# Performance work log

Measured on AMD Instinct MI355X. Metric: run time of the kernel, lower is better.

The kernel has to match this reference:

```python
import jax, jax.numpy as jnp
import numpy as np
import math

B_SZ, T_LEN = 2, 1024
D_MODEL, D_STATE, D_CONV, EXPAND = 1024, 16, 4, 2
D_INNER = EXPAND * D_MODEL            # 2048
DT_RANK = math.ceil(D_MODEL / 16)     # 64


def setup_inputs() -> dict:
    key = jax.random.key(0)
    ks = jax.random.split(key, 10)
    f32 = jnp.float32
    x = jax.random.normal(ks[0], (B_SZ, T_LEN, D_MODEL), f32)
    norm_w = jnp.ones((D_MODEL,), f32)
    in_proj_w = jax.random.normal(ks[1], (2 * D_INNER, D_MODEL), f32) / np.sqrt(D_MODEL)
    conv_w = jax.random.uniform(ks[2], (D_INNER, 1, D_CONV), f32, -0.5, 0.5)
    conv_b = jax.random.uniform(ks[3], (D_INNER,), f32, -0.5, 0.5)
    x_proj_w = jax.random.normal(ks[4], (DT_RANK + 2 * D_STATE, D_INNER), f32) / np.sqrt(D_INNER)
    dt_std = DT_RANK ** (-0.5)
    dt_proj_w = jax.random.uniform(ks[5], (D_INNER, DT_RANK), f32, -dt_std, dt_std)
    # dt bias init: softplus(bias) lands in [dt_min, dt_max]
    dt = jnp.exp(jax.random.uniform(ks[6], (D_INNER,), f32) * (np.log(0.1) - np.log(0.001)) + np.log(0.001))
    dt_proj_b = dt + jnp.log(-jnp.expm1(-dt))
    A_log = jnp.log(jnp.tile(jnp.arange(1, D_STATE + 1, dtype=f32)[None, :], (D_INNER, 1)))
    D_param = jnp.ones((D_INNER,), f32)
    out_proj_w = jax.random.normal(ks[7], (D_MODEL, D_INNER), f32) / np.sqrt(D_INNER)
    return {"x": x, "norm_w": norm_w, "in_proj_w": in_proj_w, "conv_w": conv_w,
            "conv_b": conv_b, "x_proj_w": x_proj_w, "dt_proj_w": dt_proj_w,
            "dt_proj_b": dt_proj_b, "A_log": A_log, "D_param": D_param,
            "out_proj_w": out_proj_w}


def _mamba_forward(x, norm_w, in_proj_w, conv_w, conv_b, x_proj_w,
                   dt_proj_w, dt_proj_b, A_log, D_param, out_proj_w):
    residual = x
    # RMSNorm (torch nn.RMSNorm, eps=None -> finfo eps)
    eps = jnp.finfo(x.dtype).eps
    xn = x * jax.lax.rsqrt(jnp.mean(x * x, axis=-1, keepdims=True) + eps) * norm_w
    # input projection -> ssm stream + gate
    xz = xn @ in_proj_w.T                     # [B,T,2*d_inner]
    x_s, z = xz[..., :D_INNER], xz[..., D_INNER:]
    # causal depthwise conv1d (pad left d_conv-1, matches padding=d_conv-1 then [:T])
    u = jax.lax.conv_general_dilated(
        x_s.transpose(0, 2, 1), conv_w, window_strides=(1,),
        padding=[(D_CONV - 1, 0)], dimension_numbers=("NCH", "OIH", "NCH"),
        feature_group_count=D_INNER) + conv_b[None, :, None]
    u = jax.nn.silu(u).transpose(0, 2, 1)     # [B,T,d_inner]
    # input-dependent SSM params
    x_dbc = u @ x_proj_w.T
    dt_raw = x_dbc[..., :DT_RANK]
    B_ssm = x_dbc[..., DT_RANK:DT_RANK + D_STATE]
    C_ssm = x_dbc[..., DT_RANK + D_STATE:]
    delta = jax.nn.softplus(dt_raw @ dt_proj_w.T + dt_proj_b)   # [B,T,d_inner]
    A = -jnp.exp(A_log)                                         # [d_inner,d_state]
    # discretize
    dA = jnp.exp(jnp.einsum("bti,is->btis", delta, A))          # [B,T,i,s]
    dBu = jnp.einsum("bti,bts->btis", delta * u, B_ssm)         # [B,T,i,s]
    # sequential scan over time (lax.scan, carry h [B,i,s])
    def step(h, inp):
        dA_t, dBu_t, C_t = inp
        h = dA_t * h + dBu_t
        y_t = jnp.einsum("bis,bs->bi", h, C_t)
        return h, y_t
    h0 = jnp.zeros((x.shape[0], D_INNER, D_STATE), x.dtype)
    _, ys = jax.lax.scan(step, h0,
                         (dA.transpose(1, 0, 2, 3), dBu.transpose(1, 0, 2, 3),
                          C_ssm.transpose(1, 0, 2)))
    y = ys.transpose(1, 0, 2) + u * D_param                     # [B,T,d_inner]
    y = y * jax.nn.silu(z)
    return y @ out_proj_w.T + residual


def reference(x, norm_w, in_proj_w, conv_w, conv_b, x_proj_w,
              dt_proj_w, dt_proj_b, A_log, D_param, out_proj_w):
    return _mamba_forward(x, norm_w, in_proj_w, conv_w, conv_b, x_proj_w,
                          dt_proj_w, dt_proj_b, A_log, D_param, out_proj_w)
```

## Files before the change

kernel.cpp:

```cpp
#include <hip/hip_runtime.h>
#include <math.h>

#define B_SZ 2
#define T_LEN 1024
#define D_MODEL 1024
#define D_STATE 16
#define D_INNER 2048
#define DT_RANK 64
#define NTOK (B_SZ * T_LEN)
#define XPROJ_OUT 96
#define XPROJ_LD 128
#define NCHUNK 32
#define CHUNK_L (T_LEN / NCHUNK)
#define NSPLIT 16

typedef __attribute__((ext_vector_type(8))) short bf16x8;
typedef __attribute__((ext_vector_type(4))) float f32x4;

__device__ __forceinline__ float sigmoidf_(float x) { return 1.f / (1.f + __expf(-x)); }

__device__ __forceinline__ unsigned f2bf_u(float f) {
    unsigned u = __float_as_uint(f);
    return (u + 0x7FFFu + ((u >> 16) & 1u)) >> 16;
}
__device__ __forceinline__ float bf2f(unsigned short u) {
    return __uint_as_float((unsigned)u << 16);
}

__device__ __forceinline__ void gload_lds16(const void* g, void* l) {
    __builtin_amdgcn_global_load_lds((const __attribute__((address_space(1))) unsigned*)g,
                                     (__attribute__((address_space(3))) unsigned*)l,
                                     16, 0, 0);
}

__global__ __launch_bounds__(256) void k_prep(const float* __restrict__ x,
                                              const float* __restrict__ norm_w,
                                              const float* __restrict__ w_in,
                                              const float* __restrict__ w_out,
                                              const float* __restrict__ w_x,
                                              const float* __restrict__ w_dt,
                                              unsigned short* __restrict__ xn,
                                              unsigned* __restrict__ wib,
                                              unsigned* __restrict__ wob,
                                              unsigned* __restrict__ wxb,
                                              unsigned* __restrict__ wdtb) {
    __shared__ float red[4];
    int blk = blockIdx.x;
    if (blk < 2048) {
        const float* xr = x + (size_t)blk * D_MODEL;
        int i = threadIdx.x * 4;
        float4 xv = *(const float4*)(xr + i);
        float s = xv.x * xv.x + xv.y * xv.y + xv.z * xv.z + xv.w * xv.w;
#pragma unroll
        for (int m = 1; m <= 32; m <<= 1) s += __shfl_xor(s, m);
        if ((threadIdx.x & 63) == 0) red[threadIdx.x >> 6] = s;
        __syncthreads();
        float tot = red[0] + red[1] + red[2] + red[3];
        float scale = rsqrtf(tot * (1.f / D_MODEL) + 1.1920929e-07f);
        float4 wv = *(const float4*)(norm_w + i);
        uint2 o;
        o.x = f2bf_u(xv.x * scale * wv.x) | (f2bf_u(xv.y * scale * wv.y) << 16);
        o.y = f2bf_u(xv.z * scale * wv.z) | (f2bf_u(xv.w * scale * wv.w) << 16);
        *(uint2*)(xn + (size_t)blk * D_MODEL + i) = o;
        return;
    }
    blk -= 2048;
    const float* src;
    unsigned* dst;
    int lidx;
    if (blk < 2048) {
        src = w_in; dst = wib; lidx = blk * 256 + threadIdx.x;
    } else if (blk < 3072) {
        src = w_out; dst = wob; lidx = (blk - 2048) * 256 + threadIdx.x;
    } else if (blk < 3200) {
        dst = wxb; lidx = (blk - 3072) * 256 + threadIdx.x;
        if (lidx * 8 >= 96 * 2048) {
            uint4 z = {0, 0, 0, 0};
            ((uint4*)dst)[lidx] = z;
            return;
        }
        src = w_x;
    } else {
        src = w_dt; dst = wdtb; lidx = (blk - 3200) * 256 + threadIdx.x;
    }
    float4 a = ((const float4*)src)[lidx * 2];
    float4 b = ((const float4*)src)[lidx * 2 + 1];
    uint4 o;
    o.x = f2bf_u(a.x) | (f2bf_u(a.y) << 16);
    o.y = f2bf_u(a.z) | (f2bf_u(a.w) << 16);
    o.z = f2bf_u(b.x) | (f2bf_u(b.y) << 16);
    o.w = f2bf_u(b.z) | (f2bf_u(b.w) << 16);
    ((uint4*)dst)[lidx] = o;
}


template <int BN, int CW, int EPI>
__global__ __launch_bounds__(256) void gemm_bf16(const unsigned short* __restrict__ A,
                                                 const unsigned short* __restrict__ B,
                                                 void* __restrict__ Cv, int ldc, int K,
                                                 const float* __restrict__ res) {
    constexpr int RW = 4 / CW;
    constexpr int MI = (128 / RW) / 16;
    constexpr int NJ = (BN / CW) / 16;
    __shared__ __align__(16) unsigned short As[2][128 * 64];
    __shared__ __align__(16) unsigned short Bs[2][BN * 64];
    int tid = threadIdx.x;
    int lane = tid & 63, wv = tid >> 6;
    int wr = wv / CW, wc = wv % CW;
    int lm = lane & 15, q = lane >> 4;
    int sw = lm & 7;
    int m0 = blockIdx.x * 128, n0 = blockIdx.y * BN;
    f32x4 acc[MI][NJ] = {};

    auto stage = [&](int bufi, int k0) {
#pragma unroll
        for (int it = 0; it < 4; ++it) {
            int chunk = it * 256 + tid;
            int cc = (chunk & 7) ^ ((chunk >> 3) & 7);
            const unsigned short* g = A + (size_t)(m0 + (chunk >> 3)) * K + k0 + cc * 8;
            char* l = (char*)As[bufi] + (it * 256 + wv * 64) * 16 + lane * 16;
            gload_lds16(g, l);
        }
#pragma unroll
        for (int it = 0; it < BN / 32; ++it) {
            int chunk = it * 256 + tid;
            int cc = (chunk & 7) ^ ((chunk >> 3) & 7);
            const unsigned short* g = B + (size_t)(n0 + (chunk >> 3)) * K + k0 + cc * 8;
            char* l = (char*)Bs[bufi] + (it * 256 + wv * 64) * 16 + lane * 16;
            gload_lds16(g, l);
        }
    };

    stage(0, 0);
    __syncthreads();
    int cur = 0;
    for (int k0 = 0; k0 < K; k0 += 64) {
        if (k0 + 64 < K) stage(cur ^ 1, k0 + 64);
        const unsigned short* Ac = As[cur];
        const unsigned short* Bc = Bs[cur];
#pragma unroll
        for (int h = 0; h < 2; ++h) {
            bf16x8 af[MI], bfr[NJ];
#pragma unroll
            for (int i = 0; i < MI; ++i)
                af[i] = *(const bf16x8*)(Ac + (wr * MI * 16 + i * 16 + lm) * 64 +
                                         (((h << 2) + q) ^ sw) * 8);
#pragma unroll
            for (int j = 0; j < NJ; ++j)
                bfr[j] = *(const bf16x8*)(Bc + (wc * NJ * 16 + j * 16 + lm) * 64 +
                                          (((h << 2) + q) ^ sw) * 8);
#pragma unroll
            for (int i = 0; i < MI; ++i)
#pragma unroll
                for (int j = 0; j < NJ; ++j)
                    acc[i][j] = __builtin_amdgcn_mfma_f32_16x16x32_bf16(af[i], bfr[j], acc[i][j], 0, 0, 0);
        }
        __syncthreads();
        cur ^= 1;
    }
#pragma unroll
    for (int i = 0; i < MI; ++i) {
#pragma unroll
        for (int j = 0; j < NJ; ++j) {
#pragma unroll
            for (int r = 0; r < 4; ++r) {
                int row = m0 + wr * MI * 16 + i * 16 + q * 4 + r;
                int col = n0 + wc * NJ * 16 + j * 16 + lm;
                float v = acc[i][j][r];
                if (EPI == 0) {
                    ((float*)Cv)[(size_t)row * ldc + col] = v + res[(size_t)row * ldc + col];
                } else if (EPI == 1) {
                    v += res[col];
                    v = (v > 20.f) ? v : log1pf(__expf(v));
                    ((unsigned short*)Cv)[(size_t)row * ldc + col] = (unsigned short)f2bf_u(v);
                } else {
                    if (n0 >= D_INNER) v = v * sigmoidf_(v);
                    ((unsigned short*)Cv)[(size_t)row * ldc + col] = (unsigned short)f2bf_u(v);
                }
            }
        }
    }
}

__global__ __launch_bounds__(256) void xproj_gemm(const unsigned short* __restrict__ A,
                                                  const unsigned short* __restrict__ B,
                                                  unsigned short* __restrict__ part) {
    constexpr int MI = 4, NJ = 4;
    __shared__ __align__(16) unsigned short As[2][128 * 64];
    __shared__ __align__(16) unsigned short Bs[2][128 * 64];
    int tid = threadIdx.x;
    int lane = tid & 63, wv = tid >> 6;
    int wr = wv >> 1, wc = wv & 1;
    int lm = lane & 15, q = lane >> 4;
    int sw = lm & 7;
    int m0 = blockIdx.x * 128;
    int kbase = blockIdx.y * 128;
    f32x4 acc[MI][NJ] = {};

    auto stage = [&](int bufi, int k0) {
#pragma unroll
        for (int it = 0; it < 4; ++it) {
            int chunk = it * 256 + tid;
            int cc = (chunk & 7) ^ ((chunk >> 3) & 7);
            const unsigned short* g = A + (size_t)(m0 + (chunk >> 3)) * D_INNER + k0 + cc * 8;
            char* l = (char*)As[bufi] + (it * 256 + wv * 64) * 16 + lane * 16;
            gload_lds16(g, l);
        }
#pragma unroll
        for (int it = 0; it < 4; ++it) {
            int chunk = it * 256 + tid;
            int cc = (chunk & 7) ^ ((chunk >> 3) & 7);
            const unsigned short* g = B + (size_t)(chunk >> 3) * D_INNER + k0 + cc * 8;
            char* l = (char*)Bs[bufi] + (it * 256 + wv * 64) * 16 + lane * 16;
            gload_lds16(g, l);
        }
    };

    stage(0, kbase);
    __syncthreads();
    for (int ks = 0; ks < 2; ++ks) {
        if (ks == 0) stage(1, kbase + 64);
        const unsigned short* Ac = As[ks];
        const unsigned short* Bc = Bs[ks];
#pragma unroll
        for (int h = 0; h < 2; ++h) {
            bf16x8 af[MI], bfr[NJ];
#pragma unroll
            for (int i = 0; i < MI; ++i)
                af[i] = *(const bf16x8*)(Ac + (wr * 64 + i * 16 + lm) * 64 + (((h << 2) + q) ^ sw) * 8);
#pragma unroll
            for (int j = 0; j < NJ; ++j)
                bfr[j] = *(const bf16x8*)(Bc + (wc * 64 + j * 16 + lm) * 64 + (((h << 2) + q) ^ sw) * 8);
#pragma unroll
            for (int i = 0; i < MI; ++i)
#pragma unroll
                for (int j = 0; j < NJ; ++j)
                    acc[i][j] = __builtin_amdgcn_mfma_f32_16x16x32_bf16(af[i], bfr[j], acc[i][j], 0, 0, 0);
        }
        __syncthreads();
    }
    unsigned short* dst = part + (size_t)blockIdx.y * (NTOK * XPROJ_LD);
#pragma unroll
    for (int i = 0; i < MI; ++i)
#pragma unroll
        for (int j = 0; j < NJ; ++j)
#pragma unroll
            for (int r = 0; r < 4; ++r) {
                int row = m0 + wr * 64 + i * 16 + q * 4 + r;
                int col = wc * 64 + j * 16 + lm;
                dst[(size_t)row * XPROJ_LD + col] = (unsigned short)f2bf_u(acc[i][j][r]);
            }
}

__global__ __launch_bounds__(256) void k_xred(const unsigned short* __restrict__ part,
                                              float* __restrict__ dbc,
                                              unsigned short* __restrict__ dtrawb) {
    int idx4 = blockIdx.x * 256 + threadIdx.x;
    float s0 = 0.f, s1 = 0.f, s2 = 0.f, s3 = 0.f;
#pragma unroll
    for (int sp = 0; sp < NSPLIT; ++sp) {
        uint2 v = *(const uint2*)(part + (size_t)sp * (NTOK * XPROJ_LD) + idx4 * 4);
        s0 += __uint_as_float(v.x << 16);
        s1 += __uint_as_float(v.x & 0xFFFF0000u);
        s2 += __uint_as_float(v.y << 16);
        s3 += __uint_as_float(v.y & 0xFFFF0000u);
    }
    float4 sv = {s0, s1, s2, s3};
    *(float4*)(dbc + idx4 * 4) = sv;
    int col = (idx4 * 4) & (XPROJ_LD - 1);
    if (col < DT_RANK) {
        int row = (idx4 * 4) >> 7;
        uint2 o;
        o.x = f2bf_u(s0) | (f2bf_u(s1) << 16);
        o.y = f2bf_u(s2) | (f2bf_u(s3) << 16);
        *(uint2*)(dtrawb + (size_t)row * DT_RANK + col) = o;
    }
}

__global__ __launch_bounds__(256) void k_conv(const unsigned short* __restrict__ xz,
                                              const float* __restrict__ cw,
                                              const float* __restrict__ cb,
                                              unsigned short* __restrict__ ub) {
    int idx = blockIdx.x * 256 + threadIdx.x;
    int c4 = (idx & (D_INNER / 4 - 1)) * 4;
    int t = (idx >> 9) & (T_LEN - 1);
    int b = idx >> 19;
    const unsigned short* xs = xz + (size_t)b * T_LEN * 2 * D_INNER + c4;
    float4 w[4];
#pragma unroll
    for (int i = 0; i < 4; ++i) w[i] = ((const float4*)cw)[c4 + i];
    float4 cbv = *(const float4*)(cb + c4);
    float s[4] = {cbv.x, cbv.y, cbv.z, cbv.w};
#pragma unroll
    for (int k = 0; k < 4; ++k) {
        int tt = t - 3 + k;
        if (tt >= 0) {
            ushort4 xv = *(const ushort4*)(xs + (size_t)tt * 2 * D_INNER);
            float fx0 = bf2f(xv.x), fx1 = bf2f(xv.y), fx2 = bf2f(xv.z), fx3 = bf2f(xv.w);
            float w0 = (k == 0) ? w[0].x : (k == 1) ? w[0].y : (k == 2) ? w[0].z : w[0].w;
            float w1 = (k == 0) ? w[1].x : (k == 1) ? w[1].y : (k == 2) ? w[1].z : w[1].w;
            float w2 = (k == 0) ? w[2].x : (k == 1) ? w[2].y : (k == 2) ? w[2].z : w[2].w;
            float w3 = (k == 0) ? w[3].x : (k == 1) ? w[3].y : (k == 2) ? w[3].z : w[3].w;
            s[0] = fmaf(fx0, w0, s[0]);
            s[1] = fmaf(fx1, w1, s[1]);
            s[2] = fmaf(fx2, w2, s[2]);
            s[3] = fmaf(fx3, w3, s[3]);
        }
    }
    ushort4 o;
    o.x = (unsigned short)f2bf_u(s[0] * sigmoidf_(s[0]));
    o.y = (unsigned short)f2bf_u(s[1] * sigmoidf_(s[1]));
    o.z = (unsigned short)f2bf_u(s[2] * sigmoidf_(s[2]));
    o.w = (unsigned short)f2bf_u(s[3] * sigmoidf_(s[3]));
    *(ushort4*)(ub + (size_t)(b * T_LEN + t) * D_INNER + c4) = o;
}

__global__ __launch_bounds__(256) void k_scan1(const unsigned short* __restrict__ delta,
                                               const unsigned short* __restrict__ ub,
                                               const float* __restrict__ dbc,
                                               const float* __restrict__ A_log,
                                               float* __restrict__ Pbuf,
                                               float* __restrict__ Hbuf) {
    int tid = threadIdx.x;
    int c = blockIdx.x * 256 + tid;
    int b = blockIdx.y >> 5, chunk = blockIdx.y & 31;
    int t0 = chunk * CHUNK_L;
    __shared__ float bc[CHUNK_L][32];
    {
        int t = tid >> 3, col = (tid & 7) * 4;
        const float* src = dbc + ((size_t)b * T_LEN + t0 + t) * XPROJ_LD + DT_RANK + col;
        *(float4*)&bc[t][col] = *(const float4*)src;
    }
    __syncthreads();
    float A[16];
#pragma unroll
    for (int s4 = 0; s4 < 4; ++s4) {
        float4 av = *(const float4*)(A_log + (size_t)c * D_STATE + s4 * 4);
        A[s4 * 4 + 0] = -__expf(av.x);
        A[s4 * 4 + 1] = -__expf(av.y);
        A[s4 * 4 + 2] = -__expf(av.z);
        A[s4 * 4 + 3] = -__expf(av.w);
    }
    const unsigned short* dp = delta + ((size_t)b * T_LEN + t0) * D_INNER + c;
    const unsigned short* up = ub + ((size_t)b * T_LEN + t0) * D_INNER + c;
    float h[16] = {};
    float sumd = 0.f;
#pragma unroll 4
    for (int t = 0; t < CHUNK_L; ++t) {
        float dv = bf2f(dp[(size_t)t * D_INNER]);
        float uv = bf2f(up[(size_t)t * D_INNER]);
        float du = dv * uv;
        sumd += dv;
#pragma unroll
        for (int s = 0; s < 16; ++s) {
            float da = __expf(dv * A[s]);
            h[s] = fmaf(da, h[s], du * bc[t][s]);
        }
    }
    size_t o = ((size_t)((b * NCHUNK + chunk) * D_INNER) + c) * 16;
#pragma unroll
    for (int s4 = 0; s4 < 4; ++s4) {
        float4 hv = {h[s4 * 4], h[s4 * 4 + 1], h[s4 * 4 + 2], h[s4 * 4 + 3]};
        *(float4*)(Hbuf + o + s4 * 4) = hv;
        float4 pv = {__expf(A[s4 * 4] * sumd), __expf(A[s4 * 4 + 1] * sumd),
                     __expf(A[s4 * 4 + 2] * sumd), __expf(A[s4 * 4 + 3] * sumd)};
        *(float4*)(Pbuf + o + s4 * 4) = pv;
    }
}

__global__ __launch_bounds__(256) void k_scan2(const float* __restrict__ Pbuf,
                                               const float* __restrict__ Hbuf,
                                               float* __restrict__ Sbuf) {
    int idx = blockIdx.x * 256 + threadIdx.x;
    int b = idx >> 15, r = idx & 32767;
    size_t base = (size_t)b * NCHUNK * (D_INNER * 16) + r;
    float p[NCHUNK], hl[NCHUNK];
#pragma unroll
    for (int ch = 0; ch < NCHUNK; ++ch) {
        size_t o = base + (size_t)ch * (D_INNER * 16);
        p[ch] = Pbuf[o];
        hl[ch] = Hbuf[o];
    }
    float h = 0.f;
#pragma unroll
    for (int ch = 0; ch < NCHUNK; ++ch) {
        Sbuf[base + (size_t)ch * (D_INNER * 16)] = h;
        h = fmaf(p[ch], h, hl[ch]);
    }
}

__global__ __launch_bounds__(256) void k_scan3(const unsigned short* __restrict__ delta,
                                               const unsigned short* __restrict__ ub,
                                               const float* __restrict__ dbc,
                                               const unsigned short* __restrict__ xz,
                                               const float* __restrict__ A_log,
                                               const float* __restrict__ Dp,
                                               const float* __restrict__ Sbuf,
                                               unsigned short* __restrict__ yb) {
    int tid = threadIdx.x;
    int c = blockIdx.x * 256 + tid;
    int b = blockIdx.y >> 5, chunk = blockIdx.y & 31;
    int t0 = chunk * CHUNK_L;
    __shared__ float bc[CHUNK_L][32];
    {
        int t = tid >> 3, col = (tid & 7) * 4;
        const float* src = dbc + ((size_t)b * T_LEN + t0 + t) * XPROJ_LD + DT_RANK + col;
        *(float4*)&bc[t][col] = *(const float4*)src;
    }
    __syncthreads();
    float A[16];
#pragma unroll
    for (int s4 = 0; s4 < 4; ++s4) {
        float4 av = *(const float4*)(A_log + (size_t)c * D_STATE + s4 * 4);
        A[s4 * 4 + 0] = -__expf(av.x);
        A[s4 * 4 + 1] = -__expf(av.y);
        A[s4 * 4 + 2] = -__expf(av.z);
        A[s4 * 4 + 3] = -__expf(av.w);
    }
    float Dc = Dp[c];
    float h[16];
    size_t ho = ((size_t)((b * NCHUNK + chunk) * D_INNER) + c) * 16;
#pragma unroll
    for (int s4 = 0; s4 < 4; ++s4) {
        float4 hv = *(const float4*)(Sbuf + ho + s4 * 4);
        h[s4 * 4] = hv.x; h[s4 * 4 + 1] = hv.y; h[s4 * 4 + 2] = hv.z; h[s4 * 4 + 3] = hv.w;
    }
    const unsigned short* dp = delta + ((size_t)b * T_LEN + t0) * D_INNER + c;
    const unsigned short* up = ub + ((size_t)b * T_LEN + t0) * D_INNER + c;
    const unsigned short* zp = xz + ((size_t)b * T_LEN + t0) * 2 * D_INNER + D_INNER + c;
    unsigned short* yp = yb + ((size_t)b * T_LEN + t0) * D_INNER + c;
#pragma unroll 2
    for (int t = 0; t < CHUNK_L; ++t) {
        float dv = bf2f(dp[(size_t)t * D_INNER]);
        float uv = bf2f(up[(size_t)t * D_INNER]);
        float sz = bf2f(zp[(size_t)t * 2 * D_INNER]);
        float du = dv * uv;
        float y = Dc * uv;
#pragma unroll
        for (int s = 0; s < 16; ++s) {
            float da = __expf(dv * A[s]);
            h[s] = fmaf(da, h[s], du * bc[t][s]);
            y = fmaf(h[s], bc[t][16 + s], y);
        }
        yp[(size_t)t * D_INNER] = (unsigned short)f2bf_u(y * sz);
    }
}

extern "C" void kernel_launch(void* const* d_in, const int* in_sizes, int n_in,
                              void* d_out, int out_size, void* d_ws, size_t ws_size,
                              hipStream_t stream) {
    const float* x         = (const float*)d_in[0];
    const float* norm_w    = (const float*)d_in[1];
    const float* in_proj_w = (const float*)d_in[2];
    const float* conv_w    = (const float*)d_in[3];
    const float* conv_b    = (const float*)d_in[4];
    const float* x_proj_w  = (const float*)d_in[5];
    const float* dt_proj_w = (const float*)d_in[6];
    const float* dt_proj_b = (const float*)d_in[7];
    const float* A_log     = (const float*)d_in[8];
    const float* D_param   = (const float*)d_in[9];
    const float* out_proj_w= (const float*)d_in[10];
    float* out = (float*)d_out;

    float* ws = (float*)d_ws;
    unsigned short* xzb    = (unsigned short*)(ws);
    unsigned short* ub     = (unsigned short*)(ws + 4194304);
    unsigned short* yb     = (unsigned short*)(ws + 6291456);
    unsigned short* partb  = (unsigned short*)(ws + 8388608);
    float*          dbc    = ws + 12582912;
    unsigned short* deltab = (unsigned short*)(ws + 12845056);
    float*          Pbuf   = ws + 14942208;
    float*          Hbuf   = ws + 17039360;
    float*          Sbuf   = ws + 19136512;
    unsigned short* wib    = (unsigned short*)(ws + 21233664);
    unsigned short* wob    = (unsigned short*)(ws + 23330816);
    unsigned short* wxb    = (unsigned short*)(ws + 24379392);
    unsigned short* wdtb   = (unsigned short*)(ws + 24510464);
    unsigned short* dtrawb = (unsigned short*)(ws + 24576000);
    unsigned short* xnb    = (unsigned short*)(ws + 24641536);

    k_prep<<<5312, 256, 0, stream>>>(x, norm_w, in_proj_w, out_proj_w, x_proj_w, dt_proj_w,
                                     xnb, (unsigned*)wib, (unsigned*)wob, (unsigned*)wxb,
                                     (unsigned*)wdtb);
    gemm_bf16<128, 2, 3><<<dim3(NTOK / 128, 4096 / 128), 256, 0, stream>>>(
        xnb, wib, xzb, 2 * D_INNER, D_MODEL, nullptr);
    k_conv<<<(NTOK * D_INNER / 4) / 256, 256, 0, stream>>>(xzb, conv_w, conv_b, ub);
    xproj_gemm<<<dim3(NTOK / 128, NSPLIT), 256, 0, stream>>>(ub, wxb, partb);
    k_xred<<<(NTOK * XPROJ_LD) / 1024, 256, 0, stream>>>(partb, dbc, dtrawb);
    gemm_bf16<64, 1, 1><<<dim3(NTOK / 128, D_INNER / 64), 256, 0, stream>>>(
        dtrawb, wdtb, deltab, D_INNER, DT_RANK, dt_proj_b);
    k_scan1<<<dim3(D_INNER / 256, B_SZ * NCHUNK), 256, 0, stream>>>(deltab, ub, dbc, A_log,
                                                                    Pbuf, Hbuf);
    k_scan2<<<(B_SZ * D_INNER * D_STATE) / 256, 256, 0, stream>>>(Pbuf, Hbuf, Sbuf);
    k_scan3<<<dim3(D_INNER / 256, B_SZ * NCHUNK), 256, 0, stream>>>(deltab, ub, dbc, xzb, A_log,
                                                                    D_param, Sbuf, yb);
    gemm_bf16<64, 2, 0><<<dim3(NTOK / 128, D_MODEL / 64), 256, 0, stream>>>(
        yb, wob, (void*)out, D_MODEL, D_INNER, x);

    (void)in_sizes; (void)n_in; (void)out_size; (void)ws_size;
}
```

Baseline: 252.7 us.

## Split SSM state across 4 threads per channel and stage scan inputs in LDS

The chunked scan kernels now assign four threads per channel, each owning four of the sixteen state dimensions, which gives four times as many blocks and far fewer registers per thread. Delta, u and gate values for the chunk are loaded once into shared memory with 16-byte vector loads, replacing per-timestep strided 2-byte global loads. In the output kernel the partial y values are reduced with lane shuffles and written back through shared memory as coalesced vector stores. This adds shuffle and LDS traffic per timestep, and redundant exp work for delta in exchange for higher occupancy and better memory coalescing.

```diff
diff --git a/kernel.cpp b/kernel.cpp
--- a/kernel.cpp
+++ b/kernel.cpp
@@ -322,50 +322,47 @@
                                                float* __restrict__ Pbuf,
                                                float* __restrict__ Hbuf) {
     int tid = threadIdx.x;
-    int c = blockIdx.x * 256 + tid;
+    int cl = tid >> 2, sq = tid & 3;
+    int c0 = blockIdx.x * 64;
+    int c = c0 + cl;
     int b = blockIdx.y >> 5, chunk = blockIdx.y & 31;
     int t0 = chunk * CHUNK_L;
     __shared__ float bc[CHUNK_L][32];
+    __shared__ __align__(16) unsigned short sd[CHUNK_L][64];
+    __shared__ __align__(16) unsigned short su[CHUNK_L][64];
     {
         int t = tid >> 3, col = (tid & 7) * 4;
         const float* src = dbc + ((size_t)b * T_LEN + t0 + t) * XPROJ_LD + DT_RANK + col;
         *(float4*)&bc[t][col] = *(const float4*)src;
     }
+    {
+        int r = tid >> 3, c8 = (tid & 7) * 8;
+        const unsigned short* dp0 = delta + ((size_t)b * T_LEN + t0) * D_INNER + c0;
+        const unsigned short* up0 = ub + ((size_t)b * T_LEN + t0) * D_INNER + c0;
+        *(uint4*)&sd[r][c8] = *(const uint4*)(dp0 + (size_t)r * D_INNER + c8);
+        *(uint4*)&su[r][c8] = *(const uint4*)(up0 + (size_t)r * D_INNER + c8);
+    }
     __syncthreads();
-    float A[16];
-#pragma unroll
-    for (int s4 = 0; s4 < 4; ++s4) {
-        float4 av = *(const float4*)(A_log + (size_t)c * D_STATE + s4 * 4);
-        A[s4 * 4 + 0] = -__expf(av.x);
-        A[s4 * 4 + 1] = -__expf(av.y);
-        A[s4 * 4 + 2] = -__expf(av.z);
-        A[s4 * 4 + 3] = -__expf(av.w);
-    }
-    const unsigned short* dp = delta + ((size_t)b * T_LEN + t0) * D_INNER + c;
-    const unsigned short* up = ub + ((size_t)b * T_LEN + t0) * D_INNER + c;
-    float h[16] = {};
-    float sumd = 0.f;
+    float4 av = *(const float4*)(A_log + (size_t)c * D_STATE + sq * 4);
+    float A0 = -__expf(av.x), A1 = -__expf(av.y), A2 = -__expf(av.z), A3 = -__expf(av.w);
+    float h0 = 0.f, h1 = 0.f, h2 = 0.f, h3 = 0.f, sumd = 0.f;
 #pragma unroll 4
     for (int t = 0; t < CHUNK_L; ++t) {
-        float dv = bf2f(dp[(size_t)t * D_INNER]);
-        float uv = bf2f(up[(size_t)t * D_INNER]);
+        float dv = bf2f(sd[t][cl]);
+        float uv = bf2f(su[t][cl]);
         float du = dv * uv;
         sumd += dv;
-#pragma unroll
-        for (int s = 0; s < 16; ++s) {
-            float da = __expf(dv * A[s]);
-            h[s] = fmaf(da, h[s], du * bc[t][s]);
-        }
-    }
-    size_t o = ((size_t)((b * NCHUNK + chunk) * D_INNER) + c) * 16;
-#pragma unroll
-    for (int s4 = 0; s4 < 4; ++s4) {
-        float4 hv = {h[s4 * 4], h[s4 * 4 + 1], h[s4 * 4 + 2], h[s4 * 4 + 3]};
-        *(float4*)(Hbuf + o + s4 * 4) = hv;
-        float4 pv = {__expf(A[s4 * 4] * sumd), __expf(A[s4 * 4 + 1] * sumd),
-                     __expf(A[s4 * 4 + 2] * sumd), __expf(A[s4 * 4 + 3] * sumd)};
-        *(float4*)(Pbuf + o + s4 * 4) = pv;
-    }
+        float4 Bv = *(const float4*)&bc[t][sq * 4];
+        h0 = fmaf(__expf(dv * A0), h0, du * Bv.x);
+        h1 = fmaf(__expf(dv * A1), h1, du * Bv.y);
+        h2 = fmaf(__expf(dv * A2), h2, du * Bv.z);
+        h3 = fmaf(__expf(dv * A3), h3, du * Bv.w);
+    }
+    size_t o = ((size_t)((b * NCHUNK + chunk) * D_INNER) + c) * 16 + sq * 4;
+    float4 hv = {h0, h1, h2, h3};
+    *(float4*)(Hbuf + o) = hv;
+    float4 pv = {__expf(A0 * sumd), __expf(A1 * sumd), __expf(A2 * sumd), __expf(A3 * sumd)};
+    *(float4*)(Pbuf + o) = pv;
 }
 
 __global__ __launch_bounds__(256) void k_scan2(const float* __restrict__ Pbuf,
@@ -398,51 +395,59 @@
                                                const float* __restrict__ Sbuf,
                                                unsigned short* __restrict__ yb) {
     int tid = threadIdx.x;
-    int c = blockIdx.x * 256 + tid;
+    int cl = tid >> 2, sq = tid & 3;
+    int c0 = blockIdx.x * 64;
+    int c = c0 + cl;
     int b = blockIdx.y >> 5, chunk = blockIdx.y & 31;
     int t0 = chunk * CHUNK_L;
     __shared__ float bc[CHUNK_L][32];
+    __shared__ __align__(16) unsigned short sd[CHUNK_L][64];
+    __shared__ __align__(16) unsigned short su[CHUNK_L][64];
+    __shared__ __align__(16) unsigned short szy[CHUNK_L][64];
     {
         int t = tid >> 3, col = (tid & 7) * 4;
         const float* src = dbc + ((size_t)b * T_LEN + t0 + t) * XPROJ_LD + DT_RANK + col;
         *(float4*)&bc[t][col] = *(const float4*)src;
     }
+    int r = tid >> 3, c8 = (tid & 7) * 8;
+    {
+        const unsigned short* dp0 = delta + ((size_t)b * T_LEN + t0) * D_INNER + c0;
+        const unsigned short* up0 = ub + ((size_t)b * T_LEN + t0) * D_INNER + c0;
+        const unsigned short* zp0 = xz + ((size_t)b * T_LEN + t0) * 2 * D_INNER + D_INNER + c0;
+        *(uint4*)&sd[r][c8] = *(const uint4*)(dp0 + (size_t)r * D_INNER + c8);
+        *(uint4*)&su[r][c8] = *(const uint4*)(up0 + (size_t)r * D_INNER + c8);
+        *(uint4*)&szy[r][c8] = *(const uint4*)(zp0 + (size_t)r * 2 * D_INNER + c8);
+    }
     __syncthreads();
-    float A[16];
-#pragma unroll
-    for (int s4 = 0; s4 < 4; ++s4) {
-        float4 av = *(const float4*)(A_log + (size_t)c * D_STATE + s4 * 4);
-        A[s4 * 4 + 0] = -__expf(av.x);
-        A[s4 * 4 + 1] = -__expf(av.y);
-        A[s4 * 4 + 2] = -__expf(av.z);
-        A[s4 * 4 + 3] = -__expf(av.w);
-    }
+    float4 av = *(const float4*)(A_log + (size_t)c * D_STATE + sq * 4);
+    float A0 = -__expf(av.x), A1 = -__expf(av.y), A2 = -__expf(av.z), A3 = -__expf(av.w);
     float Dc = Dp[c];
-    float h[16];
-    size_t ho = ((size_t)((b * NCHUNK + chunk) * D_INNER) + c) * 16;
-#pragma unroll
-    for (int s4 = 0; s4 < 4; ++s4) {
-        float4 hv = *(const float4*)(Sbuf + ho + s4 * 4);
-        h[s4 * 4] = hv.x; h[s4 * 4 + 1] = hv.y; h[s4 * 4 + 2] = hv.z; h[s4 * 4 + 3] = hv.w;
-    }
-    const unsigned short* dp = delta + ((size_t)b * T_LEN + t0) * D_INNER + c;
-    const unsigned short* up = ub + ((size_t)b * T_LEN + t0) * D_INNER + c;
-    const unsigned short* zp = xz + ((size_t)b * T_LEN + t0) * 2 * D_INNER + D_INNER + c;
-    unsigned short* yp = yb + ((size_t)b * T_LEN + t0) * D_INNER + c;
+    size_t ho = ((size_t)((b * NCHUNK + chunk) * D_INNER) + c) * 16 + sq * 4;
+    float4 hv = *(const float4*)(Sbuf + ho);
+    float h0 = hv.x, h1 = hv.y, h2 = hv.z, h3 = hv.w;
 #pragma unroll 2
     for (int t = 0; t < CHUNK_L; ++t) {
-        float dv = bf2f(dp[(size_t)t * D_INNER]);
-        float uv = bf2f(up[(size_t)t * D_INNER]);
-        float sz = bf2f(zp[(size_t)t * 2 * D_INNER]);
+        float dv = bf2f(sd[t][cl]);
+        float uv = bf2f(su[t][cl]);
         float du = dv * uv;
-        float y = Dc * uv;
-#pragma unroll
-        for (int s = 0; s < 16; ++s) {
-            float da = __expf(dv * A[s]);
-            h[s] = fmaf(da, h[s], du * bc[t][s]);
-            y = fmaf(h[s], bc[t][16 + s], y);
-        }
-        yp[(size_t)t * D_INNER] = (unsigned short)f2bf_u(y * sz);
+        float4 Bv = *(const float4*)&bc[t][sq * 4];
+        float4 Cv = *(const float4*)&bc[t][16 + sq * 4];
+        h0 = fmaf(__expf(dv * A0), h0, du * Bv.x);
+        h1 = fmaf(__expf(dv * A1), h1, du * Bv.y);
+        h2 = fmaf(__expf(dv * A2), h2, du * Bv.z);
+        h3 = fmaf(__expf(dv * A3), h3, du * Bv.w);
+        float yp = h0 * Cv.x + h1 * Cv.y + h2 * Cv.z + h3 * Cv.w;
+        yp += __shfl_xor(yp, 1);
+        yp += __shfl_xor(yp, 2);
+        if (sq == 0) {
+            float sz = bf2f(szy[t][cl]);
+            szy[t][cl] = (unsigned short)f2bf_u((yp + Dc * uv) * sz);
+        }
+    }
+    __syncthreads();
+    {
+        unsigned short* yp0 = yb + ((size_t)b * T_LEN + t0) * D_INNER + c0;
+        *(uint4*)(yp0 + (size_t)r * D_INNER + c8) = *(uint4*)&szy[r][c8];
     }
 }
 
@@ -489,11 +494,11 @@
     k_xred<<<(NTOK * XPROJ_LD) / 1024, 256, 0, stream>>>(partb, dbc, dtrawb);
     gemm_bf16<64, 1, 1><<<dim3(NTOK / 128, D_INNER / 64), 256, 0, stream>>>(
         dtrawb, wdtb, deltab, D_INNER, DT_RANK, dt_proj_b);
-    k_scan1<<<dim3(D_INNER / 256, B_SZ * NCHUNK), 256, 0, stream>>>(deltab, ub, dbc, A_log,
-                                                                    Pbuf, Hbuf);
+    k_scan1<<<dim3(D_INNER / 64, B_SZ * NCHUNK), 256, 0, stream>>>(deltab, ub, dbc, A_log,
+                                                                   Pbuf, Hbuf);
     k_scan2<<<(B_SZ * D_INNER * D_STATE) / 256, 256, 0, stream>>>(Pbuf, Hbuf, Sbuf);
-    k_scan3<<<dim3(D_INNER / 256, B_SZ * NCHUNK), 256, 0, stream>>>(deltab, ub, dbc, xzb, A_log,
-                                                                    D_param, Sbuf, yb);
+    k_scan3<<<dim3(D_INNER / 64, B_SZ * NCHUNK), 256, 0, stream>>>(deltab, ub, dbc, xzb, A_log,
+                                                                   D_param, Sbuf, yb);
     gemm_bf16<64, 2, 0><<<dim3(NTOK / 128, D_MODEL / 64), 256, 0, stream>>>(
         yb, wob, (void*)out, D_MODEL, D_INNER, x);
 
```

New measurement: 239.4 us. 1.06x faster.
